# Kernel tuning notes

Hardware: AMD Instinct MI355X
Metric: run time of the kernel (lower is better)

Reference implementation:

```python
import jax, jax.numpy as jnp
import numpy as np
import math

B, SQ, SK = 8, 1024, 1024
DIM_Q = DIM_K = DIM_V = 512
H = 8
EPS = 1e-5
INF = jnp.float32(1e38)


def _ln(x, g, b):
    mu = jnp.mean(x, axis=-1, keepdims=True)
    var = jnp.mean(jnp.square(x - mu), axis=-1, keepdims=True)
    return (x - mu) * jax.lax.rsqrt(var + EPS) * g + b


def setup_inputs() -> dict:
    key = jax.random.key(0)
    ks = jax.random.split(key, 12)
    s = 1.0 / math.sqrt(DIM_V)
    return {
        "queries": jax.random.normal(ks[0], (B, SQ, DIM_Q), jnp.float32),
        "keys": jax.random.normal(ks[1], (B, SK, DIM_K), jnp.float32),
        # binary presence masks (as in the original usage)
        "presence_q": (jax.random.uniform(ks[2], (B, SQ)) > 0.1).astype(jnp.float32),
        "presence_k": (jax.random.uniform(ks[3], (B, SK)) > 0.1).astype(jnp.float32),
        "num_heads": H,
        "Wq": jax.random.normal(ks[4], (DIM_Q, DIM_V), jnp.float32) * s,
        "bq": jnp.zeros((DIM_V,), jnp.float32),
        "Wk": jax.random.normal(ks[5], (DIM_K, DIM_V), jnp.float32) * s,
        "bk": jnp.zeros((DIM_V,), jnp.float32),
        "Wv": jax.random.normal(ks[6], (DIM_K, DIM_V), jnp.float32) * s,
        "bv": jnp.zeros((DIM_V,), jnp.float32),
        "Wo": jax.random.normal(ks[7], (DIM_V, DIM_V), jnp.float32) * s,
        "bo": jnp.zeros((DIM_V,), jnp.float32),
        "g0": jnp.ones((DIM_V,), jnp.float32),
        "b0": jnp.zeros((DIM_V,), jnp.float32),
        "g1": jnp.ones((DIM_V,), jnp.float32),
        "b1": jnp.zeros((DIM_V,), jnp.float32),
    }


def reference(queries, keys, presence_q, presence_k, num_heads,
              Wq, bq, Wk, bk, Wv, bv, Wo, bo, g0, b0, g1, b1):
    b, sq, _ = queries.shape
    dim_v = Wq.shape[1]
    d = dim_v // num_heads
    q = queries @ Wq + bq                              # [B,Sq,V]
    k = keys @ Wk + bk                                 # [B,Sk,V]
    v = keys @ Wv + bv                                 # [B,Sk,V]
    qh = q.reshape(b, sq, num_heads, d)
    kh = k.reshape(b, -1, num_heads, d)
    vh = v.reshape(b, -1, num_heads, d)
    logits = jnp.einsum('bqhd,bkhd->bhqk', qh, kh) / jnp.float32(math.sqrt(dim_v))
    pq = presence_q[:, None, :, None]                  # [B,1,Sq,1]
    logits = pq * logits - (1.0 - pq) * INF
    pk = presence_k[:, None, None, :]                  # [B,1,1,Sk]
    logits = pk * logits - (1.0 - pk) * INF
    A = jax.nn.softmax(logits, axis=-1)                # [B,H,Sq,Sk]
    o = qh + jnp.einsum('bhqk,bkhd->bqhd', A, vh)      # residual add of Q_
    o = o.reshape(b, sq, dim_v)
    o = _ln(o, g0, b0)
    o = o + jax.nn.relu(o @ Wo + bo)
    o = _ln(o, g1, b1)
    return o
```

## Files before the change

kernel.cpp:

```cpp
#include <hip/hip_runtime.h>

typedef __attribute__((ext_vector_type(8))) short short8;
typedef __attribute__((ext_vector_type(4))) float f32x4;

#define SCALE2 0.06375871571f

__device__ __forceinline__ float bfu(unsigned short u){
  return __uint_as_float(((unsigned int)u) << 16);
}
__device__ __forceinline__ unsigned short f2b(float x){
  unsigned int b = __float_as_uint(x);
  return (unsigned short)((b + 0x7fffu + ((b>>16)&1u)) >> 16);
}
__device__ __forceinline__ uint4 pack8(const float* f){
  float4 a = *(const float4*)f, b = *(const float4*)(f+4);
  uint4 r;
  r.x = (unsigned)f2b(a.x) | ((unsigned)f2b(a.y)<<16);
  r.y = (unsigned)f2b(a.z) | ((unsigned)f2b(a.w)<<16);
  r.z = (unsigned)f2b(b.x) | ((unsigned)f2b(b.y)<<16);
  r.w = (unsigned)f2b(b.z) | ((unsigned)f2b(b.w)<<16);
  return r;
}

__global__ __launch_bounds__(256) void prep_inputs(
    const float* Wq, const float* Wk, const float* Wv, const float* Wo,
    const float* q, const float* k, unsigned short* wt, unsigned short* qk_dst)
{
  const int id = blockIdx.x, t = threadIdx.x;
  if (id < 256){
    const int m = id >> 6;
    const float* W = (m==0)?Wq:(m==1)?Wk:(m==2)?Wv:Wo;
    unsigned short* dst = wt + (long)m*262144;
    __shared__ unsigned short tile[64][72];
    const int n0 = ((id>>3)&7)*64, k0 = (id&7)*64;
    {
      int r = t>>2, c0 = (t&3)*16;
      uint4 u0 = pack8(W + (long)(k0+r)*512 + n0 + c0);
      uint4 u1 = pack8(W + (long)(k0+r)*512 + n0 + c0 + 8);
      unsigned short* us0 = (unsigned short*)&u0;
      unsigned short* us1 = (unsigned short*)&u1;
      #pragma unroll
      for (int i=0;i<8;++i) tile[c0+i][r] = us0[i];
      #pragma unroll
      for (int i=0;i<8;++i) tile[c0+8+i][r] = us1[i];
    }
    __syncthreads();
    {
      int n = t>>2, ks = (t&3)*16;
      *(uint4*)(dst + (long)(n0+n)*512 + k0 + ks)     = *(uint4*)&tile[n][ks];
      *(uint4*)(dst + (long)(n0+n)*512 + k0 + ks + 8) = *(uint4*)&tile[n][ks+8];
    }
  } else {
    long i = ((long)(id-256)*256 + t)*8;
    const float* src = (i < 4194304) ? q + i : k + (i - 4194304);
    *(uint4*)(qk_dst + i) = pack8(src);
  }
}

__global__ __launch_bounds__(256) void proj_mfma(
    const unsigned short* qin, const unsigned short* kin, const unsigned short* wt,
    const float* bq, const float* bk, const float* bv,
    unsigned short* q_bf, unsigned short* k_bf, unsigned short* vt_bf)
{
  const int mat = blockIdx.z;
  const unsigned short* A = (mat==0)? qin : kin;
  const unsigned short* Wt = wt + (long)mat*262144;
  const float* bias = (mat==0)?bq:(mat==1)?bk:bv;
  const int row0 = blockIdx.y*128, col0 = blockIdx.x*128;
  __shared__ unsigned short As[2][128][40];
  __shared__ unsigned short Ws[2][128][40];
  const int t = threadIdx.x;
  const int lane = t & 63, wid = t >> 6;
  const int ln = lane & 15, quad = lane >> 4;
  const int wy = wid >> 1, wx = wid & 1;
  f32x4 acc[4][4];
  #pragma unroll
  for (int i=0;i<4;++i){
    #pragma unroll
    for (int j=0;j<4;++j) acc[i][j] = (f32x4){0.f,0.f,0.f,0.f};
  }
  const int sr = t>>1, sk0 = (t&1)*16;
  const unsigned short* Arow = A  + (long)(row0+sr)*512 + sk0;
  const unsigned short* Wrow = Wt + (long)(col0+sr)*512 + sk0;
  uint4 a0 = *(const uint4*)(Arow);
  uint4 a1 = *(const uint4*)(Arow + 8);
  uint4 w0 = *(const uint4*)(Wrow);
  uint4 w1 = *(const uint4*)(Wrow + 8);
  *(uint4*)&As[0][sr][sk0]   = a0;
  *(uint4*)&As[0][sr][sk0+8] = a1;
  *(uint4*)&Ws[0][sr][sk0]   = w0;
  *(uint4*)&Ws[0][sr][sk0+8] = w1;
  __syncthreads();
  for (int it=0; it<16; ++it){
    const int cur = it & 1;
    if (it < 15){
      a0 = *(const uint4*)(Arow + (it+1)*32);
      a1 = *(const uint4*)(Arow + (it+1)*32 + 8);
      w0 = *(const uint4*)(Wrow + (it+1)*32);
      w1 = *(const uint4*)(Wrow + (it+1)*32 + 8);
    }
    short8 a[4], b[4];
    #pragma unroll
    for (int mt=0;mt<4;++mt) a[mt] = *(const short8*)&As[cur][wy*64+mt*16+ln][quad*8];
    #pragma unroll
    for (int nt=0;nt<4;++nt) b[nt] = *(const short8*)&Ws[cur][wx*64+nt*16+ln][quad*8];
    #pragma unroll
    for (int mt=0;mt<4;++mt){
      #pragma unroll
      for (int nt=0;nt<4;++nt)
        acc[mt][nt] = __builtin_amdgcn_mfma_f32_16x16x32_bf16(a[mt], b[nt], acc[mt][nt], 0,0,0);
    }
    if (it < 15){
      *(uint4*)&As[cur^1][sr][sk0]   = a0;
      *(uint4*)&As[cur^1][sr][sk0+8] = a1;
      *(uint4*)&Ws[cur^1][sr][sk0]   = w0;
      *(uint4*)&Ws[cur^1][sr][sk0+8] = w1;
    }
    __syncthreads();
  }
  float bias_v[4];
  #pragma unroll
  for (int nt=0;nt<4;++nt) bias_v[nt] = bias[col0 + wx*64 + nt*16 + ln];
  if (mat < 2){
    unsigned short* dst = (mat==0)? q_bf : k_bf;
    #pragma unroll
    for (int mt=0;mt<4;++mt){
      int row = row0 + wy*64 + mt*16 + quad*4;
      #pragma unroll
      for (int nt=0;nt<4;++nt){
        int col = col0 + wx*64 + nt*16 + ln;
        #pragma unroll
        for (int r=0;r<4;++r)
          dst[(long)(row+r)*512 + col] = f2b(acc[mt][nt][r] + bias_v[nt]);
      }
    }
  } else {
    #pragma unroll
    for (int mt=0;mt<4;++mt){
      int row = row0 + wy*64 + mt*16 + quad*4;
      int bb = row >> 10, sk = row & 1023;
      #pragma unroll
      for (int nt=0;nt<4;++nt){
        int col = col0 + wx*64 + nt*16 + ln;
        int h = col >> 6, dd = col & 63;
        uint2 pk2; unsigned short* pp = (unsigned short*)&pk2;
        #pragma unroll
        for (int r=0;r<4;++r) pp[r] = f2b(acc[mt][nt][r] + bias_v[nt]);
        *(uint2*)(vt_bf + (((long)((bb*8+h)*64+dd)) << 10) + sk) = pk2;
      }
    }
  }
}

__global__ __launch_bounds__(512, 4) void attn_mfma(
    const unsigned short* q_bf, const unsigned short* k_bf, const unsigned short* vt_bf,
    const float* pres_q, const float* pres_k, unsigned short* o_bf)
{
  const int bx = blockIdx.x;
  const int b = bx >> 3, h = bx & 7;
  const int q0 = blockIdx.y * 128;
  const int t = threadIdx.x;
  const int lane = t & 63, wid = t >> 6, ln = lane & 15, quad = lane >> 4;
  const int g = wid >> 1, khalf = wid & 1;

  __shared__ unsigned short Ks[128][72];
  __shared__ unsigned short Vt[64][136];
  __shared__ unsigned short Pw[8][16][72];
  __shared__ float pk_s[128];

  const unsigned short* Kg = k_bf  + ((long)b*1024)*512 + h*64;
  const unsigned short* Vg = vt_bf + (((long)(b*8+h)) << 16);
  const float* pkg = pres_k + b*1024;

  const int krow = t >> 2, kcol = (t & 3) * 16;
  const int vrow = t >> 3, vcol = (t & 7) * 16;

  {
    uint4 ka = *(const uint4*)(Kg + (long)krow*512 + kcol);
    uint4 kb = *(const uint4*)(Kg + (long)krow*512 + kcol + 8);
    uint4 va = *(const uint4*)(Vg + (long)vrow*1024 + vcol);
    uint4 vb = *(const uint4*)(Vg + (long)vrow*1024 + vcol + 8);
    *(uint4*)&Ks[krow][kcol]   = ka;
    *(uint4*)&Ks[krow][kcol+8] = kb;
    *(uint4*)&Vt[vrow][vcol]   = va;
    *(uint4*)&Vt[vrow][vcol+8] = vb;
    if (t < 128) pk_s[t] = pkg[t];
  }

  short8 aq[2][2]; float av[2], mval[2];
  #pragma unroll
  for (int st=0;st<2;++st){
    int qi = q0 + g*32 + st*16 + ln;
    const unsigned short* qrow = q_bf + ((long)(b*1024 + qi))*512 + h*64;
    aq[st][0] = *(const short8*)(qrow + quad*8);
    aq[st][1] = *(const short8*)(qrow + 32 + quad*8);
    av[st]   = SCALE2 * pres_q[b*1024 + qi];
    mval[st] = (av[st] == 0.f) ? 0.f : -43.f;
  }
  f32x4 oacc[2][4];
  #pragma unroll
  for (int st=0;st<2;++st){
    #pragma unroll
    for (int i=0;i<4;++i) oacc[st][i] = (f32x4){0.f,0.f,0.f,0.f};
  }
  float lsum[2] = {0.f, 0.f};
  __syncthreads();

  const int tb = khalf * 64;
  for (int s=0; s<8; ++s){
    uint4 pka, pkb, pva, pvb; float ppk = 0.f;
    if (s < 7){
      const long off = (long)(s+1)*128;
      pka = *(const uint4*)(Kg + (off + krow)*512 + kcol);
      pkb = *(const uint4*)(Kg + (off + krow)*512 + kcol + 8);
      pva = *(const uint4*)(Vg + (long)vrow*1024 + off + vcol);
      pvb = *(const uint4*)(Vg + (long)vrow*1024 + off + vcol + 8);
      if (t < 128) ppk = pkg[off + t];
    }
    #pragma unroll
    for (int st=0; st<2; ++st){
      f32x4 sc[4];
      #pragma unroll
      for (int kt=0;kt<4;++kt) sc[kt] = (f32x4){0.f,0.f,0.f,0.f};
      __builtin_amdgcn_s_setprio(1);
      #pragma unroll
      for (int kt=0;kt<4;++kt){
        short8 kb0 = *(const short8*)&Ks[tb + kt*16+ln][quad*8];
        short8 kb1 = *(const short8*)&Ks[tb + kt*16+ln][32+quad*8];
        sc[kt] = __builtin_amdgcn_mfma_f32_16x16x32_bf16(kb0, aq[st][0], sc[kt], 0,0,0);
        sc[kt] = __builtin_amdgcn_mfma_f32_16x16x32_bf16(kb1, aq[st][1], sc[kt], 0,0,0);
      }
      __builtin_amdgcn_s_setprio(0);
      #pragma unroll
      for (int kt=0;kt<4;++kt){
        float4 pk4 = *(const float4*)&pk_s[tb + kt*16 + quad*4];
        float x0 = __builtin_fmaf(pk4.x, __builtin_fmaf(sc[kt][0], av[st], -mval[st]), mval[st]);
        float x1 = __builtin_fmaf(pk4.y, __builtin_fmaf(sc[kt][1], av[st], -mval[st]), mval[st]);
        float x2 = __builtin_fmaf(pk4.z, __builtin_fmaf(sc[kt][2], av[st], -mval[st]), mval[st]);
        float x3 = __builtin_fmaf(pk4.w, __builtin_fmaf(sc[kt][3], av[st], -mval[st]), mval[st]);
        float e0 = __builtin_amdgcn_exp2f(x0);
        float e1 = __builtin_amdgcn_exp2f(x1);
        float e2 = __builtin_amdgcn_exp2f(x2);
        float e3 = __builtin_amdgcn_exp2f(x3);
        lsum[st] += (e0+e1)+(e2+e3);
        uint2 w;
        w.x = (unsigned)f2b(e0) | ((unsigned)f2b(e1)<<16);
        w.y = (unsigned)f2b(e2) | ((unsigned)f2b(e3)<<16);
        *(uint2*)&Pw[wid][ln][kt*16 + quad*4] = w;
      }
      short8 ap0 = *(const short8*)&Pw[wid][ln][quad*8];
      short8 ap1 = *(const short8*)&Pw[wid][ln][32 + quad*8];
      __builtin_amdgcn_s_setprio(1);
      #pragma unroll
      for (int dt=0;dt<4;++dt){
        short8 vb0 = *(const short8*)&Vt[dt*16+ln][tb + quad*8];
        short8 vb1 = *(const short8*)&Vt[dt*16+ln][tb + 32 + quad*8];
        oacc[st][dt] = __builtin_amdgcn_mfma_f32_16x16x32_bf16(ap0, vb0, oacc[st][dt], 0,0,0);
        oacc[st][dt] = __builtin_amdgcn_mfma_f32_16x16x32_bf16(ap1, vb1, oacc[st][dt], 0,0,0);
      }
      __builtin_amdgcn_s_setprio(0);
    }
    __syncthreads();
    if (s < 7){
      *(uint4*)&Ks[krow][kcol]   = pka;
      *(uint4*)&Ks[krow][kcol+8] = pkb;
      *(uint4*)&Vt[vrow][vcol]   = pva;
      *(uint4*)&Vt[vrow][vcol+8] = pvb;
      if (t < 128) pk_s[t] = ppk;
      __syncthreads();
    }
  }

  float* MSf = (float*)&Pw[0][0][0];
  #pragma unroll
  for (int st=0; st<2; ++st){
    __syncthreads();
    if (khalf == 1){
      float* m = MSf + (g*64 + lane)*18;
      #pragma unroll
      for (int dt=0;dt<4;++dt){
        #pragma unroll
        for (int r=0;r<4;++r) m[dt*4+r] = oacc[st][dt][r];
      }
      m[16] = lsum[st];
    }
    __syncthreads();
    if (khalf == 0){
      const float* m = MSf + (g*64 + lane)*18;
      float l = lsum[st] + m[16];
      #pragma unroll
      for (int dt=0;dt<4;++dt){
        #pragma unroll
        for (int r=0;r<4;++r) oacc[st][dt][r] += m[dt*4+r];
      }
      l += __shfl_xor(l, 16);
      l += __shfl_xor(l, 32);
      #pragma unroll
      for (int r=0;r<4;++r){
        float lr = __shfl(l, quad*4 + r);
        float inv = 1.f / lr;
        int ql = q0 + g*32 + st*16 + quad*4 + r;
        long base = ((long)(b*1024 + ql))*512 + h*64;
        #pragma unroll
        for (int dt=0;dt<4;++dt){
          float qh = bfu(q_bf[base + dt*16 + ln]);
          o_bf[base + dt*16 + ln] = f2b(qh + oacc[st][dt][r]*inv);
        }
      }
    }
  }
}

__global__ __launch_bounds__(256) void ln_kernel(
    const unsigned short* in, void* outp, int mode, const float* g, const float* bvec)
{
  const int row = blockIdx.x*4 + (threadIdx.x >> 6);
  const int lane = threadIdx.x & 63;
  uint4 raw = *(const uint4*)(in + (long)row*512 + lane*8);
  const unsigned short* rs16 = (const unsigned short*)&raw;
  float v[8];
  #pragma unroll
  for (int c=0;c<8;++c) v[c] = bfu(rs16[c]);
  float sum = 0.f;
  #pragma unroll
  for (int c=0;c<8;++c) sum += v[c];
  #pragma unroll
  for (int msk=1; msk<64; msk<<=1) sum += __shfl_xor(sum, msk);
  float mu = sum * (1.f/512.f);
  float var = 0.f;
  #pragma unroll
  for (int c=0;c<8;++c){ v[c] -= mu; var += v[c]*v[c]; }
  #pragma unroll
  for (int msk=1; msk<64; msk<<=1) var += __shfl_xor(var, msk);
  float rs = rsqrtf(var*(1.f/512.f) + 1e-5f);
  float gv[8], bv[8];
  *(float4*)&gv[0] = *(const float4*)(g + lane*8);
  *(float4*)&gv[4] = *(const float4*)(g + lane*8 + 4);
  *(float4*)&bv[0] = *(const float4*)(bvec + lane*8);
  *(float4*)&bv[4] = *(const float4*)(bvec + lane*8 + 4);
  float y[8];
  #pragma unroll
  for (int c=0;c<8;++c) y[c] = v[c]*rs*gv[c] + bv[c];
  if (mode){
    float* dst = (float*)outp + (long)row*512 + lane*8;
    *(float4*)dst       = *(float4*)&y[0];
    *(float4*)(dst + 4) = *(float4*)&y[4];
  } else {
    uint4 out; unsigned short* os = (unsigned short*)&out;
    #pragma unroll
    for (int c=0;c<8;++c) os[c] = f2b(y[c]);
    *(uint4*)((unsigned short*)outp + (long)row*512 + lane*8) = out;
  }
}

__global__ __launch_bounds__(256) void out_mfma(
    const unsigned short* t_bf, const unsigned short* Wt, const float* bo,
    unsigned short* u_bf)
{
  const int row0 = blockIdx.y*64, col0 = blockIdx.x*128;
  __shared__ unsigned short As[2][64][40];
  __shared__ unsigned short Ws[2][128][40];
  const int t = threadIdx.x;
  const int lane = t & 63, wid = t >> 6;
  const int ln = lane & 15, quad = lane >> 4;
  const int wy = wid >> 1, wx = wid & 1;
  f32x4 acc[2][4];
  #pragma unroll
  for (int i=0;i<2;++i){
    #pragma unroll
    for (int j=0;j<4;++j) acc[i][j] = (f32x4){0.f,0.f,0.f,0.f};
  }
  const int ar = t>>2, ac0 = (t&3)*8;
  const int wr = t>>1, wc0 = (t&1)*16;
  const unsigned short* Arow = t_bf + (long)(row0+ar)*512 + ac0;
  const unsigned short* Wrow = Wt   + (long)(col0+wr)*512 + wc0;
  uint4 a0 = *(const uint4*)(Arow);
  uint4 w0 = *(const uint4*)(Wrow);
  uint4 w1 = *(const uint4*)(Wrow + 8);
  *(uint4*)&As[0][ar][ac0] = a0;
  *(uint4*)&Ws[0][wr][wc0]   = w0;
  *(uint4*)&Ws[0][wr][wc0+8] = w1;
  __syncthreads();
  for (int it=0; it<16; ++it){
    const int cur = it & 1;
    if (it < 15){
      a0 = *(const uint4*)(Arow + (it+1)*32);
      w0 = *(const uint4*)(Wrow + (it+1)*32);
      w1 = *(const uint4*)(Wrow + (it+1)*32 + 8);
    }
    short8 a[2], b[4];
    #pragma unroll
    for (int mt=0;mt<2;++mt) a[mt] = *(const short8*)&As[cur][wy*32+mt*16+ln][quad*8];
    #pragma unroll
    for (int nt=0;nt<4;++nt) b[nt] = *(const short8*)&Ws[cur][wx*64+nt*16+ln][quad*8];
    #pragma unroll
    for (int mt=0;mt<2;++mt){
      #pragma unroll
      for (int nt=0;nt<4;++nt)
        acc[mt][nt] = __builtin_amdgcn_mfma_f32_16x16x32_bf16(a[mt], b[nt], acc[mt][nt], 0,0,0);
    }
    if (it < 15){
      *(uint4*)&As[cur^1][ar][ac0] = a0;
      *(uint4*)&Ws[cur^1][wr][wc0]   = w0;
      *(uint4*)&Ws[cur^1][wr][wc0+8] = w1;
    }
    __syncthreads();
  }
  float bias_v[4];
  #pragma unroll
  for (int nt=0;nt<4;++nt) bias_v[nt] = bo[col0 + wx*64 + nt*16 + ln];
  #pragma unroll
  for (int mt=0;mt<2;++mt){
    int row = row0 + wy*32 + mt*16 + quad*4;
    #pragma unroll
    for (int nt=0;nt<4;++nt){
      int col = col0 + wx*64 + nt*16 + ln;
      #pragma unroll
      for (int r=0;r<4;++r){
        long idx = (long)(row+r)*512 + col;
        float u = acc[mt][nt][r] + bias_v[nt];
        u = fmaxf(u, 0.f);
        u_bf[idx] = f2b(bfu(t_bf[idx]) + u);
      }
    }
  }
}

extern "C" void kernel_launch(void* const* d_in, const int* in_sizes, int n_in,
                              void* d_out, int out_size, void* d_ws, size_t ws_size,
                              hipStream_t stream)
{
  unsigned short* q_bf  = (unsigned short*)d_ws;
  unsigned short* k_bf  = q_bf  + 8192l*512;
  unsigned short* vt_bf = k_bf  + 8192l*512;
  unsigned short* t_bf  = vt_bf + 8192l*512;
  unsigned short* wt    = t_bf  + 8192l*512;
  unsigned short* qin   = wt + 4l*512*512;
  unsigned short* kin   = qin + 4194304;
  unsigned short* o_bf  = qin;
  unsigned short* u_bf  = kin;

  hipLaunchKernelGGL(prep_inputs, dim3(4352), dim3(256), 0, stream,
                     (const float*)d_in[5], (const float*)d_in[7],
                     (const float*)d_in[9], (const float*)d_in[11],
                     (const float*)d_in[0], (const float*)d_in[1], wt, qin);
  hipLaunchKernelGGL(proj_mfma, dim3(4,64,3), dim3(256), 0, stream,
                     qin, kin, wt,
                     (const float*)d_in[6], (const float*)d_in[8],
                     (const float*)d_in[10], q_bf, k_bf, vt_bf);
  hipLaunchKernelGGL(attn_mfma, dim3(64,8), dim3(512), 0, stream,
                     q_bf, k_bf, vt_bf,
                     (const float*)d_in[2], (const float*)d_in[3], o_bf);
  hipLaunchKernelGGL(ln_kernel, dim3(2048), dim3(256), 0, stream,
                     o_bf, (void*)t_bf, 0, (const float*)d_in[13], (const float*)d_in[14]);
  hipLaunchKernelGGL(out_mfma, dim3(4,128), dim3(256), 0, stream,
                     t_bf, wt + 3l*512*512, (const float*)d_in[12], u_bf);
  hipLaunchKernelGGL(ln_kernel, dim3(2048), dim3(256), 0, stream,
                     u_bf, d_out, 1, (const float*)d_in[15], (const float*)d_in[16]);
}
```

Measured before the change: 222.3 us.

## Share K/V fragment loads across both query subtiles in attention loop

Restructures the per-tile attention loop so that each K and V fragment read from LDS feeds MFMAs for both 16-row query subtiles, rather than re-reading it once per subtile. The P buffer doubles so both subtiles' probabilities are staged at once. Launch bounds drop from 4 to 2 waves per SIMD, letting the compiler use more registers for the extra live score and fragment state. This cuts LDS traffic and gives more independent MFMAs to interleave, at the cost of occupancy and more shared memory.

```diff
diff --git a/kernel.cpp b/kernel.cpp
--- a/kernel.cpp
+++ b/kernel.cpp
@@ -152,7 +152,7 @@
   }
 }
 
-__global__ __launch_bounds__(512, 4) void attn_mfma(
+__global__ __launch_bounds__(512, 2) void attn_mfma(
     const unsigned short* q_bf, const unsigned short* k_bf, const unsigned short* vt_bf,
     const float* pres_q, const float* pres_k, unsigned short* o_bf)
 {
@@ -165,7 +165,7 @@
 
   __shared__ unsigned short Ks[128][72];
   __shared__ unsigned short Vt[64][136];
-  __shared__ unsigned short Pw[8][16][72];
+  __shared__ unsigned short Pw[8][32][72];
   __shared__ float pk_s[128];
 
   const unsigned short* Kg = k_bf  + ((long)b*1024)*512 + h*64;
@@ -217,27 +217,32 @@
       pvb = *(const uint4*)(Vg + (long)vrow*1024 + off + vcol + 8);
       if (t < 128) ppk = pkg[off + t];
     }
-    #pragma unroll
-    for (int st=0; st<2; ++st){
-      f32x4 sc[4];
-      #pragma unroll
-      for (int kt=0;kt<4;++kt) sc[kt] = (f32x4){0.f,0.f,0.f,0.f};
-      __builtin_amdgcn_s_setprio(1);
-      #pragma unroll
-      for (int kt=0;kt<4;++kt){
-        short8 kb0 = *(const short8*)&Ks[tb + kt*16+ln][quad*8];
-        short8 kb1 = *(const short8*)&Ks[tb + kt*16+ln][32+quad*8];
-        sc[kt] = __builtin_amdgcn_mfma_f32_16x16x32_bf16(kb0, aq[st][0], sc[kt], 0,0,0);
-        sc[kt] = __builtin_amdgcn_mfma_f32_16x16x32_bf16(kb1, aq[st][1], sc[kt], 0,0,0);
-      }
-      __builtin_amdgcn_s_setprio(0);
+    f32x4 sc[2][4];
+    #pragma unroll
+    for (int st=0;st<2;++st){
+      #pragma unroll
+      for (int kt=0;kt<4;++kt) sc[st][kt] = (f32x4){0.f,0.f,0.f,0.f};
+    }
+    __builtin_amdgcn_s_setprio(1);
+    #pragma unroll
+    for (int kt=0;kt<4;++kt){
+      short8 kb0 = *(const short8*)&Ks[tb + kt*16+ln][quad*8];
+      short8 kb1 = *(const short8*)&Ks[tb + kt*16+ln][32+quad*8];
+      sc[0][kt] = __builtin_amdgcn_mfma_f32_16x16x32_bf16(kb0, aq[0][0], sc[0][kt], 0,0,0);
+      sc[0][kt] = __builtin_amdgcn_mfma_f32_16x16x32_bf16(kb1, aq[0][1], sc[0][kt], 0,0,0);
+      sc[1][kt] = __builtin_amdgcn_mfma_f32_16x16x32_bf16(kb0, aq[1][0], sc[1][kt], 0,0,0);
+      sc[1][kt] = __builtin_amdgcn_mfma_f32_16x16x32_bf16(kb1, aq[1][1], sc[1][kt], 0,0,0);
+    }
+    __builtin_amdgcn_s_setprio(0);
+    #pragma unroll
+    for (int st=0;st<2;++st){
       #pragma unroll
       for (int kt=0;kt<4;++kt){
         float4 pk4 = *(const float4*)&pk_s[tb + kt*16 + quad*4];
-        float x0 = __builtin_fmaf(pk4.x, __builtin_fmaf(sc[kt][0], av[st], -mval[st]), mval[st]);
-        float x1 = __builtin_fmaf(pk4.y, __builtin_fmaf(sc[kt][1], av[st], -mval[st]), mval[st]);
-        float x2 = __builtin_fmaf(pk4.z, __builtin_fmaf(sc[kt][2], av[st], -mval[st]), mval[st]);
-        float x3 = __builtin_fmaf(pk4.w, __builtin_fmaf(sc[kt][3], av[st], -mval[st]), mval[st]);
+        float x0 = __builtin_fmaf(pk4.x, __builtin_fmaf(sc[st][kt][0], av[st], -mval[st]), mval[st]);
+        float x1 = __builtin_fmaf(pk4.y, __builtin_fmaf(sc[st][kt][1], av[st], -mval[st]), mval[st]);
+        float x2 = __builtin_fmaf(pk4.z, __builtin_fmaf(sc[st][kt][2], av[st], -mval[st]), mval[st]);
+        float x3 = __builtin_fmaf(pk4.w, __builtin_fmaf(sc[st][kt][3], av[st], -mval[st]), mval[st]);
         float e0 = __builtin_amdgcn_exp2f(x0);
         float e1 = __builtin_amdgcn_exp2f(x1);
         float e2 = __builtin_amdgcn_exp2f(x2);
@@ -246,20 +251,26 @@
         uint2 w;
         w.x = (unsigned)f2b(e0) | ((unsigned)f2b(e1)<<16);
         w.y = (unsigned)f2b(e2) | ((unsigned)f2b(e3)<<16);
-        *(uint2*)&Pw[wid][ln][kt*16 + quad*4] = w;
-      }
-      short8 ap0 = *(const short8*)&Pw[wid][ln][quad*8];
-      short8 ap1 = *(const short8*)&Pw[wid][ln][32 + quad*8];
-      __builtin_amdgcn_s_setprio(1);
-      #pragma unroll
-      for (int dt=0;dt<4;++dt){
-        short8 vb0 = *(const short8*)&Vt[dt*16+ln][tb + quad*8];
-        short8 vb1 = *(const short8*)&Vt[dt*16+ln][tb + 32 + quad*8];
-        oacc[st][dt] = __builtin_amdgcn_mfma_f32_16x16x32_bf16(ap0, vb0, oacc[st][dt], 0,0,0);
-        oacc[st][dt] = __builtin_amdgcn_mfma_f32_16x16x32_bf16(ap1, vb1, oacc[st][dt], 0,0,0);
-      }
-      __builtin_amdgcn_s_setprio(0);
-    }
+        *(uint2*)&Pw[wid][st*16+ln][kt*16 + quad*4] = w;
+      }
+    }
+    short8 ap[2][2];
+    #pragma unroll
+    for (int st=0;st<2;++st){
+      ap[st][0] = *(const short8*)&Pw[wid][st*16+ln][quad*8];
+      ap[st][1] = *(const short8*)&Pw[wid][st*16+ln][32 + quad*8];
+    }
+    __builtin_amdgcn_s_setprio(1);
+    #pragma unroll
+    for (int dt=0;dt<4;++dt){
+      short8 vb0 = *(const short8*)&Vt[dt*16+ln][tb + quad*8];
+      short8 vb1 = *(const short8*)&Vt[dt*16+ln][tb + 32 + quad*8];
+      oacc[0][dt] = __builtin_amdgcn_mfma_f32_16x16x32_bf16(ap[0][0], vb0, oacc[0][dt], 0,0,0);
+      oacc[0][dt] = __builtin_amdgcn_mfma_f32_16x16x32_bf16(ap[0][1], vb1, oacc[0][dt], 0,0,0);
+      oacc[1][dt] = __builtin_amdgcn_mfma_f32_16x16x32_bf16(ap[1][0], vb0, oacc[1][dt], 0,0,0);
+      oacc[1][dt] = __builtin_amdgcn_mfma_f32_16x16x32_bf16(ap[1][1], vb1, oacc[1][dt], 0,0,0);
+    }
+    __builtin_amdgcn_s_setprio(0);
     __syncthreads();
     if (s < 7){
       *(uint4*)&Ks[krow][kcol]   = pka;
```

New measurement: 216.7 us. 2.5% less time.
